# Optimization experiments

Hardware: AMD Instinct MI355X
Metric: run time of the kernel (lower is better)

## Reference

```python
import jax, jax.numpy as jnp
import numpy as np

N_HEADS = 16
HIDDEN = 1024
HEAD = HIDDEN // N_HEADS


def setup_inputs() -> dict:
    key = jax.random.key(0)
    ks = jax.random.split(key, 11)
    B, S, H = 2, 2048, HIDDEN
    s = 1.0 / np.sqrt(H)
    return {
        "query": jax.random.normal(ks[0], (B, S, H), jnp.float32),
        "key": jax.random.normal(ks[1], (B, S, H), jnp.float32),
        "value": jax.random.normal(ks[2], (B, S, H), jnp.float32),
        "Wq": jax.random.normal(ks[3], (H, H), jnp.float32) * s,
        "bq": jnp.zeros((H,), jnp.float32),
        "Wk": jax.random.normal(ks[4], (H, H), jnp.float32) * s,
        "bk": jnp.zeros((H,), jnp.float32),
        "Wv": jax.random.normal(ks[5], (H, H), jnp.float32) * s,
        "bv": jnp.zeros((H,), jnp.float32),
        "Wo": jax.random.normal(ks[6], (H, H), jnp.float32) * s,
        "bo": jnp.zeros((H,), jnp.float32),
    }


def reference(query, key, value, Wq, bq, Wk, bk, Wv, bv, Wo, bo):
    B, Sq, H = query.shape
    Sk = key.shape[1]
    # QKV projections, split heads: [B, n_heads, S, head]
    q = (query @ Wq + bq).reshape(B, Sq, N_HEADS, HEAD).transpose(0, 2, 1, 3)
    k = (key @ Wk + bk).reshape(B, Sk, N_HEADS, HEAD).transpose(0, 2, 1, 3)
    v = (value @ Wv + bv).reshape(B, Sk, N_HEADS, HEAD).transpose(0, 2, 1, 3)
    # scaled dot-product attention (no mask, dropout p=0)
    scores = jnp.einsum("bhqd,bhkd->bhqk", q, k) / np.sqrt(HEAD).astype(np.float32)
    attn = jax.nn.softmax(scores, axis=-1)
    out = jnp.einsum("bhqk,bhkd->bhqd", attn, v)
    out = out.transpose(0, 2, 1, 3).reshape(B, Sq, H)
    return out @ Wo + bo
```

## Files before the change

### kernel.cpp

```cpp
#include <hip/hip_runtime.h>
#include <hip/hip_bf16.h>
#include <stdint.h>

typedef unsigned short u16;
typedef short bf16x8 __attribute__((ext_vector_type(8)));
typedef float f32x4 __attribute__((ext_vector_type(4)));

#define DEVI static __device__ __forceinline__

#if __has_builtin(__builtin_amdgcn_exp2f)
#define EXP2F(x) __builtin_amdgcn_exp2f(x)
#else
#define EXP2F(x) exp2f(x)
#endif

DEVI u16 f2bf(float f) {
  union { float f; uint32_t u; } v; v.f = f;
  uint32_t u = v.u;
  u += 0x7fffu + ((u >> 16) & 1u);
  return (u16)(u >> 16);
}
DEVI uint32_t pk2bf(float lo, float hi) {
  __hip_bfloat162 h = __float22bfloat162_rn(float2{lo, hi});
  union { __hip_bfloat162 h; uint32_t u; } v; v.h = h; return v.u;
}

DEVI void async16(const void* g, const void* l) {
  __builtin_amdgcn_global_load_lds(
      (const __attribute__((address_space(1))) void*)g,
      (__attribute__((address_space(3))) void*)l, 16, 0, 0);
}

DEVI f32x4 mfma16(bf16x8 a, bf16x8 b, f32x4 c) {
  return __builtin_amdgcn_mfma_f32_16x16x32_bf16(a, b, c, 0, 0, 0);
}

#define CSC 0.18033688011112042f

__global__ void prep(const float* __restrict__ q, const float* __restrict__ k,
                     const float* __restrict__ v,
                     const float* __restrict__ Wq, const float* __restrict__ Wk,
                     const float* __restrict__ Wv, const float* __restrict__ Wo,
                     u16* __restrict__ XB, u16* __restrict__ WT) {
  __shared__ u16 tile[64 * 68];
  const int bid = blockIdx.x, t = threadIdx.x;
  if (bid < 12288) {
    const int z = bid >> 12, x = bid & 4095;
    const float* src = (z == 0) ? q : (z == 1) ? k : v;
    const int i = (x * 256 + t) * 4;
    float4 f = *(const float4*)(src + i);
    ushort4 o;
    o.x = f2bf(f.x); o.y = f2bf(f.y); o.z = f2bf(f.z); o.w = f2bf(f.w);
    *(ushort4*)(XB + (size_t)z * 4194304 + i) = o;
  } else {
    const int j = bid - 12288;
    const int z = j >> 8, rem = j & 255;
    const float* W = (z == 0) ? Wq : (z == 1) ? Wk : (z == 2) ? Wv : Wo;
    u16* out = WT + (size_t)z * 1048576;
    const int R0 = (rem >> 4) * 64, C0 = (rem & 15) * 64;
#pragma unroll
    for (int it = 0; it < 16; ++it) {
      int jj = it * 256 + t;
      int r = jj >> 6, c = jj & 63;
      tile[r * 68 + c] = f2bf(W[(size_t)(R0 + r) * 1024 + C0 + c]);
    }
    __syncthreads();
#pragma unroll
    for (int it = 0; it < 16; ++it) {
      int jj = it * 256 + t;
      int c = jj >> 6, r = jj & 63;
      out[(size_t)(C0 + c) * 1024 + R0 + r] = tile[r * 68 + c];
    }
  }
}

__global__ __launch_bounds__(256, 3)
void qkv_gemm(const u16* __restrict__ XB, const u16* __restrict__ WT,
              const float* __restrict__ bq, const float* __restrict__ bk,
              const float* __restrict__ bv,
              u16* __restrict__ QN, u16* __restrict__ KN, u16* __restrict__ VT) {
  __shared__ u16 smem[16896];
  const int z = blockIdx.y;
  const u16* A  = XB + (size_t)z * 4194304;
  const u16* Bt = WT + (size_t)z * 1048576;
  const float* bias = (z == 0) ? bq : (z == 1) ? bk : bv;
  const int T = blockIdx.x;
  const int m0 = (T & 31) * 128, n0 = (T >> 5) * 128;
  const int t = threadIdx.x, lane = t & 63, w = t >> 6;
  const int quad = lane >> 4, l16 = lane & 15;
  const int wm = (w & 1) * 64, wn = (w >> 1) * 64;

#define QSTAGE32(k0, buf)                                                     \
  do {                                                                        \
    u16* lA_ = smem + (buf) * 8192;                                           \
    u16* lB_ = lA_ + 4096;                                                    \
    _Pragma("unroll")                                                         \
    for (int half = 0; half < 2; ++half) {                                    \
      int i = half * 256 + t;                                                 \
      int r = i >> 2, cc = i & 3, c = cc ^ ((r >> 1) & 3);                    \
      async16(A + (size_t)(m0 + r) * 1024 + (k0) + c * 8, &lA_[i * 8]);       \
      async16(Bt + (size_t)(n0 + r) * 1024 + (k0) + c * 8, &lB_[i * 8]);      \
    }                                                                         \
  } while (0)

  QSTAGE32(0, 0);

  f32x4 acc[4][4] = {};
  for (int kt = 0; kt < 32; ++kt) {
    asm volatile("s_waitcnt vmcnt(0)" ::: "memory");
    __builtin_amdgcn_s_barrier();
    __builtin_amdgcn_sched_barrier(0);
    if (kt + 1 < 32) QSTAGE32((kt + 1) * 32, (kt + 1) & 1);
    const u16* lA = smem + (kt & 1) * 8192;
    const u16* lB = lA + 4096;
    bf16x8 af[4], bfr[4];
#pragma unroll
    for (int rt = 0; rt < 4; ++rt) {
      int row = wm + rt * 16 + l16;
      af[rt] = *(const bf16x8*)&lA[row * 32 + (quad ^ ((row >> 1) & 3)) * 8];
    }
#pragma unroll
    for (int ct = 0; ct < 4; ++ct) {
      int row = wn + ct * 16 + l16;
      bfr[ct] = *(const bf16x8*)&lB[row * 32 + (quad ^ ((row >> 1) & 3)) * 8];
    }
    __builtin_amdgcn_s_setprio(1);
#pragma unroll
    for (int rt = 0; rt < 4; ++rt)
#pragma unroll
      for (int ct = 0; ct < 4; ++ct)
        acc[rt][ct] = mfma16(bfr[ct], af[rt], acc[rt][ct]);
    __builtin_amdgcn_s_setprio(0);
  }
#undef QSTAGE32
  __syncthreads();

  if (z < 2) {
    const float scl = (z == 0) ? CSC : 1.0f;
#pragma unroll
    for (int rt = 0; rt < 4; ++rt) {
      int sl = wm + rt * 16 + l16;
#pragma unroll
      for (int ct = 0; ct < 4; ++ct) {
        int nb = wn + ct * 16 + quad * 4;
        float4 b4 = *(const float4*)&bias[n0 + nb];
        ushort4 pk;
        pk.x = f2bf((acc[rt][ct][0] + b4.x) * scl);
        pk.y = f2bf((acc[rt][ct][1] + b4.y) * scl);
        pk.z = f2bf((acc[rt][ct][2] + b4.z) * scl);
        pk.w = f2bf((acc[rt][ct][3] + b4.w) * scl);
        *(ushort4*)&smem[sl * 132 + nb] = pk;
      }
    }
    __syncthreads();
    u16* out = (z == 0) ? QN : KN;
#pragma unroll
    for (int p = 0; p < 8; ++p) {
      int idx = p * 256 + t;
      int row = idx >> 4, chunk = idx & 15;
      *(bf16x8*)&out[(size_t)(m0 + row) * 1024 + n0 + chunk * 8] =
          *(const bf16x8*)&smem[row * 132 + chunk * 8];
    }
  } else {
#pragma unroll
    for (int rt = 0; rt < 4; ++rt) {
      int sl = wm + rt * 16 + l16;
#pragma unroll
      for (int ct = 0; ct < 4; ++ct) {
        int nb = wn + ct * 16 + quad * 4;
        float4 b4 = *(const float4*)&bias[n0 + nb];
        smem[(nb + 0) * 132 + sl] = f2bf(acc[rt][ct][0] + b4.x);
        smem[(nb + 1) * 132 + sl] = f2bf(acc[rt][ct][1] + b4.y);
        smem[(nb + 2) * 132 + sl] = f2bf(acc[rt][ct][2] + b4.z);
        smem[(nb + 3) * 132 + sl] = f2bf(acc[rt][ct][3] + b4.w);
      }
    }
    __syncthreads();
    const int bb = m0 >> 11, sb = m0 & 2047;
#pragma unroll
    for (int p = 0; p < 8; ++p) {
      int idx = p * 256 + t;
      int dl = idx >> 4, chunk = idx & 15;
      int ncol = n0 + dl, hh = ncol >> 6, dd = ncol & 63;
      *(bf16x8*)&VT[((size_t)((bb * 16 + hh) * 64 + dd)) * 2048 + sb + chunk * 8] =
          *(const bf16x8*)&smem[dl * 132 + chunk * 8];
    }
  }
}

__global__ __launch_bounds__(512, 4)
void attn11(const u16* __restrict__ QN, const u16* __restrict__ KN,
            const u16* __restrict__ VT, u16* __restrict__ AO) {
  __shared__ u16 lK[4][64 * 64];
  __shared__ u16 lV[4][64 * 64];
  const int qt0 = blockIdx.x, h = blockIdx.y, b = blockIdx.z;
  const int t = threadIdx.x, lane = t & 63, w = t >> 6;
  const int quad = lane >> 4, l16 = lane & 15;
  const u16* Qg = QN + ((size_t)(b * 2048 + qt0 * 128)) * 1024 + h * 64;
  const u16* Kg = KN + ((size_t)b * 2048) * 1024 + h * 64;
  const u16* Vg = VT + ((size_t)((b * 16 + h) * 64)) * 2048;

  const int sr_r = t >> 3;
  const int sg_r = (sr_r & 0x23) | ((sr_r & 8) << 1) | ((sr_r & 4) << 1) |
                   ((sr_r & 16) >> 2);
  const int sc_c = (t & 7) ^ (sr_r & 7);

  bf16x8 qf[2];
#pragma unroll
  for (int ks = 0; ks < 2; ++ks)
    qf[ks] = *(const bf16x8*)(Qg + (size_t)(w * 16 + l16) * 1024 + ks * 32 + quad * 8);

  const bf16x8 ones = {0x3F80, 0x3F80, 0x3F80, 0x3F80,
                       0x3F80, 0x3F80, 0x3F80, 0x3F80};

  async16(Kg + (size_t)sg_r * 1024 + sc_c * 8, &lK[0][t * 8]);
  async16(Vg + (size_t)sr_r * 2048 + sc_c * 8, &lV[0][t * 8]);
  async16(Kg + (size_t)(64 + sg_r) * 1024 + sc_c * 8, &lK[1][t * 8]);
  async16(Vg + (size_t)sr_r * 2048 + 64 + sc_c * 8, &lV[1][t * 8]);

  f32x4 o[4] = {};
  f32x4 ls = {};

  for (int it = 0; it < 16; ++it) {
    const int ta = it * 2;
    asm volatile("s_waitcnt vmcnt(0)" ::: "memory");
    __builtin_amdgcn_s_barrier();
    __builtin_amdgcn_sched_barrier(0);

    if (it + 1 < 16) {
      const int kb0 = (ta + 2) * 64, nb0 = (ta + 2) & 3;
      async16(Kg + (size_t)(kb0 + sg_r) * 1024 + sc_c * 8, &lK[nb0][t * 8]);
      async16(Vg + (size_t)sr_r * 2048 + kb0 + sc_c * 8, &lV[nb0][t * 8]);
      const int kb1 = (ta + 3) * 64, nb1 = (ta + 3) & 3;
      async16(Kg + (size_t)(kb1 + sg_r) * 1024 + sc_c * 8, &lK[nb1][t * 8]);
      async16(Vg + (size_t)sr_r * 2048 + kb1 + sc_c * 8, &lV[nb1][t * 8]);
    }

    f32x4 sc2[2][4];
    __builtin_amdgcn_s_setprio(1);
#pragma unroll
    for (int u = 0; u < 2; ++u) {
      const u16* Kc = &lK[(ta + u) & 3][0];
#pragma unroll
      for (int st = 0; st < 4; ++st) {
        int row = st * 16 + l16;
        bf16x8 kf0 = *(const bf16x8*)&Kc[row * 64 + ((quad) ^ (row & 7)) * 8];
        bf16x8 kf1 = *(const bf16x8*)&Kc[row * 64 + ((4 + quad) ^ (row & 7)) * 8];
        f32x4 z = {};
        sc2[u][st] = mfma16(kf0, qf[0], z);
        sc2[u][st] = mfma16(kf1, qf[1], sc2[u][st]);
      }
    }
    __builtin_amdgcn_s_setprio(0);

#pragma unroll
    for (int u = 0; u < 2; ++u) {
      union { uint32_t uw[4]; bf16x8 v; } p0, p1;
#pragma unroll
      for (int st = 0; st < 2; ++st) {
        p0.uw[st * 2 + 0] = pk2bf(EXP2F(sc2[u][st][0]), EXP2F(sc2[u][st][1]));
        p0.uw[st * 2 + 1] = pk2bf(EXP2F(sc2[u][st][2]), EXP2F(sc2[u][st][3]));
        p1.uw[st * 2 + 0] = pk2bf(EXP2F(sc2[u][2 + st][0]), EXP2F(sc2[u][2 + st][1]));
        p1.uw[st * 2 + 1] = pk2bf(EXP2F(sc2[u][2 + st][2]), EXP2F(sc2[u][2 + st][3]));
      }
      __builtin_amdgcn_s_setprio(1);
      ls = mfma16(ones, p0.v, ls);
      ls = mfma16(ones, p1.v, ls);
      const u16* Vc = &lV[(ta + u) & 3][0];
#pragma unroll
      for (int dt = 0; dt < 4; ++dt) {
        int row = dt * 16 + l16;
        bf16x8 vf0 = *(const bf16x8*)&Vc[row * 64 + ((quad) ^ (row & 7)) * 8];
        bf16x8 vf1 = *(const bf16x8*)&Vc[row * 64 + ((4 + quad) ^ (row & 7)) * 8];
        o[dt] = mfma16(vf0, p0.v, o[dt]);
        o[dt] = mfma16(vf1, p1.v, o[dt]);
      }
      __builtin_amdgcn_s_setprio(0);
    }
  }

  float inv = 1.0f / ls[0];
  int qglob = qt0 * 128 + w * 16 + l16;
  size_t base = ((size_t)(b * 2048 + qglob)) * 1024 + h * 64;
#pragma unroll
  for (int dt = 0; dt < 4; ++dt) {
    ushort4 pk;
    pk.x = f2bf(o[dt][0] * inv);
    pk.y = f2bf(o[dt][1] * inv);
    pk.z = f2bf(o[dt][2] * inv);
    pk.w = f2bf(o[dt][3] * inv);
    *(ushort4*)&AO[base + dt * 16 + quad * 4] = pk;
  }
}

__global__ __launch_bounds__(256, 3)
void oproj_gemm(const u16* __restrict__ AO, const u16* __restrict__ Bt,
                const float* __restrict__ bias, float* __restrict__ out) {
  __shared__ u16 smem[24576];
  const int T = blockIdx.x;
  const int m0 = (T & 31) * 128, n0 = (T >> 5) * 64;
  const int t = threadIdx.x, lane = t & 63, w = t >> 6;
  const int quad = lane >> 4, l16 = lane & 15;
  const int wm = (w & 1) * 64, wn = (w >> 1) * 32;

  {
    u16* lA = smem; u16* lB = smem + 8192;
#pragma unroll
    for (int it = 0; it < 4; ++it) {
      int i = it * 256 + t;
      int r = i >> 3, cc = i & 7, c = cc ^ (r & 7);
      async16(AO + (size_t)(m0 + r) * 1024 + c * 8, &lA[i * 8]);
    }
#pragma unroll
    for (int it = 0; it < 2; ++it) {
      int i = it * 256 + t;
      int r = i >> 3, cc = i & 7, c = cc ^ (r & 7);
      async16(Bt + (size_t)(n0 + r) * 1024 + c * 8, &lB[i * 8]);
    }
  }

  f32x4 acc[4][2] = {};
  for (int kt = 0; kt < 16; ++kt) {
    asm volatile("s_waitcnt vmcnt(0)" ::: "memory");
    __builtin_amdgcn_s_barrier();
    __builtin_amdgcn_sched_barrier(0);
    if (kt + 1 < 16) {
      const int k0 = (kt + 1) * 64;
      u16* lA = smem + ((kt + 1) & 1) * 12288;
      u16* lB = lA + 8192;
#pragma unroll
      for (int it = 0; it < 4; ++it) {
        int i = it * 256 + t;
        int r = i >> 3, cc = i & 7, c = cc ^ (r & 7);
        async16(AO + (size_t)(m0 + r) * 1024 + k0 + c * 8, &lA[i * 8]);
      }
#pragma unroll
      for (int it = 0; it < 2; ++it) {
        int i = it * 256 + t;
        int r = i >> 3, cc = i & 7, c = cc ^ (r & 7);
        async16(Bt + (size_t)(n0 + r) * 1024 + k0 + c * 8, &lB[i * 8]);
      }
    }
    const u16* lA = smem + (kt & 1) * 12288;
    const u16* lB = lA + 8192;
#pragma unroll
    for (int ks = 0; ks < 2; ++ks) {
      bf16x8 af[4], bfr[2];
#pragma unroll
      for (int rt = 0; rt < 4; ++rt) {
        int row = wm + rt * 16 + l16;
        af[rt] = *(const bf16x8*)&lA[row * 64 + ((ks * 4 + quad) ^ (row & 7)) * 8];
      }
#pragma unroll
      for (int ct = 0; ct < 2; ++ct) {
        int row = wn + ct * 16 + l16;
        bfr[ct] = *(const bf16x8*)&lB[row * 64 + ((ks * 4 + quad) ^ (row & 7)) * 8];
      }
      __builtin_amdgcn_s_setprio(1);
#pragma unroll
      for (int rt = 0; rt < 4; ++rt)
#pragma unroll
        for (int ct = 0; ct < 2; ++ct)
          acc[rt][ct] = mfma16(af[rt], bfr[ct], acc[rt][ct]);
      __builtin_amdgcn_s_setprio(0);
    }
  }

#pragma unroll
  for (int ct = 0; ct < 2; ++ct) {
    int ncol = n0 + wn + ct * 16 + l16;
    float bvv = bias[ncol];
#pragma unroll
    for (int rt = 0; rt < 4; ++rt)
#pragma unroll
      for (int r = 0; r < 4; ++r) {
        int m = m0 + wm + rt * 16 + quad * 4 + r;
        out[(size_t)m * 1024 + ncol] = acc[rt][ct][r] + bvv;
      }
  }
}

extern "C" void kernel_launch(void* const* d_in, const int* in_sizes, int n_in,
                              void* d_out, int out_size, void* d_ws, size_t ws_size,
                              hipStream_t stream) {
  const float* query = (const float*)d_in[0];
  const float* key   = (const float*)d_in[1];
  const float* value = (const float*)d_in[2];
  const float* Wq = (const float*)d_in[3];
  const float* bq = (const float*)d_in[4];
  const float* Wk = (const float*)d_in[5];
  const float* bk = (const float*)d_in[6];
  const float* Wv = (const float*)d_in[7];
  const float* bv = (const float*)d_in[8];
  const float* Wo = (const float*)d_in[9];
  const float* bo = (const float*)d_in[10];
  float* out = (float*)d_out;

  u16* WT = (u16*)d_ws;
  u16* QN = WT + 4 * 1048576;
  u16* KN = QN + 4194304;
  u16* VT = KN + 4194304;
  u16* XB = VT + 4194304;
  u16* AO = XB;

  prep<<<dim3(13312), 256, 0, stream>>>(query, key, value, Wq, Wk, Wv, Wo, XB, WT);
  qkv_gemm<<<dim3(256, 3), 256, 0, stream>>>(XB, WT, bq, bk, bv, QN, KN, VT);
  attn11<<<dim3(16, 16, 2), 512, 0, stream>>>(QN, KN, VT, AO);
  oproj_gemm<<<dim3(512), 256, 0, stream>>>(AO, WT + 3 * 1048576, bo, out);
}
```

Measured before the change: 206.9 us.

## Switch QKV and output-projection GEMMs to triple-buffered LDS pipelines

The QKV GEMM moves from double to triple buffering. It issues the next stage's async loads before waiting and uses a partial vmcnt wait, so one stage of loads stays in flight during compute. The output-projection GEMM does the same, and also drops its K-tile from 64 to 32 with a matching swizzle. That shrinks its shared memory, so launch bounds rise to 4 blocks per CU. The exchange is more loop iterations and barriers in oproj, plus a larger LDS footprint for the QKV kernel.

```diff
diff --git a/kernel.cpp b/kernel.cpp
--- a/kernel.cpp
+++ b/kernel.cpp
@@ -79,7 +79,7 @@
               const float* __restrict__ bq, const float* __restrict__ bk,
               const float* __restrict__ bv,
               u16* __restrict__ QN, u16* __restrict__ KN, u16* __restrict__ VT) {
-  __shared__ u16 smem[16896];
+  __shared__ u16 smem[24576];
   const int z = blockIdx.y;
   const u16* A  = XB + (size_t)z * 4194304;
   const u16* Bt = WT + (size_t)z * 1048576;
@@ -106,12 +106,18 @@
   QSTAGE32(0, 0);
 
   f32x4 acc[4][4] = {};
+  int cur = 0;
   for (int kt = 0; kt < 32; ++kt) {
-    asm volatile("s_waitcnt vmcnt(0)" ::: "memory");
+    const int nxt = (cur == 2) ? 0 : cur + 1;
+    if (kt + 1 < 32) {
+      QSTAGE32((kt + 1) * 32, nxt);
+      asm volatile("s_waitcnt vmcnt(4)" ::: "memory");
+    } else {
+      asm volatile("s_waitcnt vmcnt(0)" ::: "memory");
+    }
     __builtin_amdgcn_s_barrier();
     __builtin_amdgcn_sched_barrier(0);
-    if (kt + 1 < 32) QSTAGE32((kt + 1) * 32, (kt + 1) & 1);
-    const u16* lA = smem + (kt & 1) * 8192;
+    const u16* lA = smem + cur * 8192;
     const u16* lB = lA + 4096;
     bf16x8 af[4], bfr[4];
 #pragma unroll
@@ -131,6 +137,7 @@
       for (int ct = 0; ct < 4; ++ct)
         acc[rt][ct] = mfma16(bfr[ct], af[rt], acc[rt][ct]);
     __builtin_amdgcn_s_setprio(0);
+    cur = nxt;
   }
 #undef QSTAGE32
   __syncthreads();
@@ -293,78 +300,69 @@
   }
 }
 
-__global__ __launch_bounds__(256, 3)
+__global__ __launch_bounds__(256, 4)
 void oproj_gemm(const u16* __restrict__ AO, const u16* __restrict__ Bt,
                 const float* __restrict__ bias, float* __restrict__ out) {
-  __shared__ u16 smem[24576];
+  __shared__ u16 smem[18432];
   const int T = blockIdx.x;
   const int m0 = (T & 31) * 128, n0 = (T >> 5) * 64;
   const int t = threadIdx.x, lane = t & 63, w = t >> 6;
   const int quad = lane >> 4, l16 = lane & 15;
   const int wm = (w & 1) * 64, wn = (w >> 1) * 32;
 
-  {
-    u16* lA = smem; u16* lB = smem + 8192;
-#pragma unroll
-    for (int it = 0; it < 4; ++it) {
-      int i = it * 256 + t;
-      int r = i >> 3, cc = i & 7, c = cc ^ (r & 7);
-      async16(AO + (size_t)(m0 + r) * 1024 + c * 8, &lA[i * 8]);
-    }
-#pragma unroll
-    for (int it = 0; it < 2; ++it) {
-      int i = it * 256 + t;
-      int r = i >> 3, cc = i & 7, c = cc ^ (r & 7);
-      async16(Bt + (size_t)(n0 + r) * 1024 + c * 8, &lB[i * 8]);
-    }
-  }
+#define OSTAGE32(k0, buf)                                                     \
+  do {                                                                        \
+    u16* lA_ = smem + (buf) * 6144;                                           \
+    u16* lB_ = lA_ + 4096;                                                    \
+    _Pragma("unroll")                                                         \
+    for (int half = 0; half < 2; ++half) {                                    \
+      int i = half * 256 + t;                                                 \
+      int r = i >> 2, cc = i & 3, c = cc ^ ((r >> 1) & 3);                    \
+      async16(AO + (size_t)(m0 + r) * 1024 + (k0) + c * 8, &lA_[i * 8]);      \
+    }                                                                         \
+    {                                                                         \
+      int r = t >> 2, cc = t & 3, c = cc ^ ((r >> 1) & 3);                    \
+      async16(Bt + (size_t)(n0 + r) * 1024 + (k0) + c * 8, &lB_[t * 8]);      \
+    }                                                                         \
+  } while (0)
+
+  OSTAGE32(0, 0);
 
   f32x4 acc[4][2] = {};
-  for (int kt = 0; kt < 16; ++kt) {
-    asm volatile("s_waitcnt vmcnt(0)" ::: "memory");
+  int cur = 0;
+  for (int kt = 0; kt < 32; ++kt) {
+    const int nxt = (cur == 2) ? 0 : cur + 1;
+    if (kt + 1 < 32) {
+      OSTAGE32((kt + 1) * 32, nxt);
+      asm volatile("s_waitcnt vmcnt(3)" ::: "memory");
+    } else {
+      asm volatile("s_waitcnt vmcnt(0)" ::: "memory");
+    }
     __builtin_amdgcn_s_barrier();
     __builtin_amdgcn_sched_barrier(0);
-    if (kt + 1 < 16) {
-      const int k0 = (kt + 1) * 64;
-      u16* lA = smem + ((kt + 1) & 1) * 12288;
-      u16* lB = lA + 8192;
-#pragma unroll
-      for (int it = 0; it < 4; ++it) {
-        int i = it * 256 + t;
-        int r = i >> 3, cc = i & 7, c = cc ^ (r & 7);
-        async16(AO + (size_t)(m0 + r) * 1024 + k0 + c * 8, &lA[i * 8]);
-      }
-#pragma unroll
-      for (int it = 0; it < 2; ++it) {
-        int i = it * 256 + t;
-        int r = i >> 3, cc = i & 7, c = cc ^ (r & 7);
-        async16(Bt + (size_t)(n0 + r) * 1024 + k0 + c * 8, &lB[i * 8]);
-      }
-    }
-    const u16* lA = smem + (kt & 1) * 12288;
-    const u16* lB = lA + 8192;
-#pragma unroll
-    for (int ks = 0; ks < 2; ++ks) {
-      bf16x8 af[4], bfr[2];
-#pragma unroll
-      for (int rt = 0; rt < 4; ++rt) {
-        int row = wm + rt * 16 + l16;
-        af[rt] = *(const bf16x8*)&lA[row * 64 + ((ks * 4 + quad) ^ (row & 7)) * 8];
-      }
-#pragma unroll
-      for (int ct = 0; ct < 2; ++ct) {
-        int row = wn + ct * 16 + l16;
-        bfr[ct] = *(const bf16x8*)&lB[row * 64 + ((ks * 4 + quad) ^ (row & 7)) * 8];
-      }
-      __builtin_amdgcn_s_setprio(1);
-#pragma unroll
-      for (int rt = 0; rt < 4; ++rt)
-#pragma unroll
-        for (int ct = 0; ct < 2; ++ct)
-          acc[rt][ct] = mfma16(af[rt], bfr[ct], acc[rt][ct]);
-      __builtin_amdgcn_s_setprio(0);
-    }
-  }
+    const u16* lA = smem + cur * 6144;
+    const u16* lB = lA + 4096;
+    bf16x8 af[4], bfr[2];
+#pragma unroll
+    for (int rt = 0; rt < 4; ++rt) {
+      int row = wm + rt * 16 + l16;
+      af[rt] = *(const bf16x8*)&lA[row * 32 + (quad ^ ((row >> 1) & 3)) * 8];
+    }
+#pragma unroll
+    for (int ct = 0; ct < 2; ++ct) {
+      int row = wn + ct * 16 + l16;
+      bfr[ct] = *(const bf16x8*)&lB[row * 32 + (quad ^ ((row >> 1) & 3)) * 8];
+    }
+    __builtin_amdgcn_s_setprio(1);
+#pragma unroll
+    for (int rt = 0; rt < 4; ++rt)
+#pragma unroll
+      for (int ct = 0; ct < 2; ++ct)
+        acc[rt][ct] = mfma16(af[rt], bfr[ct], acc[rt][ct]);
+    __builtin_amdgcn_s_setprio(0);
+    cur = nxt;
+  }
+#undef OSTAGE32
 
 #pragma unroll
   for (int ct = 0; ct < 2; ++ct) {
```

Result: slower. 212.7 us (+2.8%).
